# Kernel tuning notes

Hardware: AMD Instinct MI355X
Metric: run time of the kernel (lower is better)

The kernel has to match this reference:

```python
import jax, jax.numpy as jnp
import numpy as np

B, S, DIN, D, H, DK, FF, V, L = 4, 1024, 768, 224, 8, 28, 600, 8000, 8


def setup_inputs() -> dict:
    key = jax.random.key(0)
    ks = iter(jax.random.split(key, 32))
    g = lambda shape, s=0.02: jax.random.normal(next(ks), shape, jnp.float32) * s
    return {
        "x": jax.random.normal(next(ks), (B, S, DIN), jnp.float32),
        "Wp": g((DIN, D)), "bp": jnp.zeros((D,), jnp.float32),
        # per-layer stacked params, leading axis = L layers
        "Wq": g((L, H, D, DK)), "bq": jnp.zeros((L, H, DK), jnp.float32),
        "Wk": g((L, H, D, DK)), "bk": jnp.zeros((L, H, DK), jnp.float32),
        "Wv": g((L, H, D, DK)), "bv": jnp.zeros((L, H, DK), jnp.float32),
        "Wo": g((L, D, D)), "bo": jnp.zeros((L, D), jnp.float32),
        "W1": g((L, D, FF)), "b1": jnp.zeros((L, FF), jnp.float32),
        "W2": g((L, FF, FF)), "b2": jnp.zeros((L, FF), jnp.float32),
        "W3": g((L, FF, D)), "b3": jnp.zeros((L, D), jnp.float32),
        # LayerNorm over last TWO dims (seq, dmodel), one shared instance per layer
        "lnw": jnp.ones((L, S, D), jnp.float32), "lnb": jnp.zeros((L, S, D), jnp.float32),
        "Wf": g((D, V)), "bf": jnp.zeros((V,), jnp.float32),
    }


def _pos_enc(S_, D_):
    pos = jnp.arange(S_, dtype=jnp.float32)[:, None]          # [S,1]
    i = jnp.arange(D_, dtype=jnp.float32)[None, :]            # [1,D]
    ang = pos / jnp.power(jnp.float32(10000.0), 2.0 * i / D_)  # uses 2*i for BOTH
    return jnp.where(jnp.arange(D_)[None, :] % 2 == 0, jnp.sin(ang), jnp.cos(ang))


def _ln2d(x, w, b):
    # LayerNorm over last two dims (seq, dmodel), eps=1e-5
    mu = jnp.mean(x, axis=(-2, -1), keepdims=True)
    var = jnp.var(x, axis=(-2, -1), keepdims=True)
    return (x - mu) / jnp.sqrt(var + 1e-5) * w + b


def _attn(x, Wq, bq, Wk, bk, Wv, bv, Wo, bo):
    q = jnp.einsum('bsd,hdk->bhsk', x, Wq) + bq[:, None, :]
    k = jnp.einsum('bsd,hdk->bhsk', x, Wk) + bk[:, None, :]
    v = jnp.einsum('bsd,hdk->bhsk', x, Wv) + bv[:, None, :]
    scores = jnp.einsum('bhqk,bhsk->bhqs', q, k) / jnp.sqrt(jnp.float32(DK))
    causal = jnp.tril(jnp.ones((S, S), bool))
    scores = jnp.where(causal, scores, -jnp.inf)
    a = jax.nn.softmax(scores, axis=-1)
    o = jnp.einsum('bhqs,bhsk->bqhk', a, v).reshape(x.shape[0], S, D)
    return o @ Wo + bo + x  # residual inside attention (as in source)


def reference(x, Wp, bp, Wq, bq, Wk, bk, Wv, bv, Wo, bo,
              W1, b1, W2, b2, W3, b3, lnw, lnb, Wf, bf):
    h = x @ Wp + bp                      # proj_to_224: [B,S,224]
    h = h + _pos_enc(S, D)[None]         # positional encoding
    for l in range(L):
        h = _attn(h, Wq[l], bq[l], Wk[l], bk[l], Wv[l], bv[l], Wo[l], bo[l])
        h = _ln2d(h, lnw[l], lnb[l])
        f = jax.nn.relu(h @ W1[l] + b1[l])
        f = jax.nn.relu(f @ W2[l] + b2[l])
        f = f @ W3[l] + b3[l]
        h = _ln2d(f + h, lnw[l], lnb[l])  # feed_forward's LN (same params)
        h = _ln2d(h, lnw[l], lnb[l])      # outer LN (same params again)
    logits = (h @ Wf + bf) / 1.0          # temperature = 1.0
    return jax.nn.softmax(logits, axis=2)
```

## Files before the change

### kernel.cpp

```cpp
#include <hip/hip_runtime.h>
#include <math.h>

#define GF_BIAS   1
#define GF_RELU   2
#define GF_RESID  4
#define GF_POSENC 8
#define GF_F32OUT 16
#define GF_STAT6  32
#define GF_SWAP   64
#define GF_LNA    128
#define GF_LNA2   256
#define GF_LNRES  512
#define GF_LNRES2 1024

namespace {
constexpr int BB = 4, SS = 1024, DD = 224, FFF = 600, VV = 8000, LLl = 8;
constexpr int SD = SS * DD;
constexpr float INV_SD = 1.0f / (float)SD;

constexpr size_t WP   = 0;
constexpr size_t WQKV = WP + (size_t)256 * 768;
constexpr size_t WO   = WQKV + (size_t)LLl * 704 * 256;
constexpr size_t W1T  = WO + (size_t)LLl * 256 * 256;
constexpr size_t W2T  = W1T + (size_t)LLl * 640 * 256;
constexpr size_t W3T  = W2T + (size_t)LLl * 640 * 640;
constexpr size_t WFT  = W3T + (size_t)LLl * 256 * 640;
constexpr size_t HB   = WFT + (size_t)8064 * 256;
constexpr size_t H2B  = HB + (size_t)4096 * 256;
constexpr size_t OBUF = H2B + (size_t)4096 * 256;
constexpr size_t BIG  = OBUF + (size_t)4096 * 256;
constexpr size_t ENDB = BIG + (size_t)2 * 4096 * 640;
constexpr size_t FBYTE = ENDB * 2;
}

using short8 = __attribute__((ext_vector_type(8))) short;
using f32x4  = __attribute__((ext_vector_type(4))) float;

__device__ __forceinline__ float bits2f(unsigned u) {
  union { unsigned u; float f; } v; v.u = u; return v.f;
}
__device__ __forceinline__ unsigned short f2b(float f) {
  union { float f; unsigned u; } v; v.f = f;
  unsigned r = v.u + 0x7FFFu + ((v.u >> 16) & 1u);
  return (unsigned short)(r >> 16);
}
__device__ __forceinline__ float b2f(unsigned short b) {
  return bits2f((unsigned)b << 16);
}

__device__ __forceinline__ uint4 ln8(uint4 raw, const float* __restrict__ wp,
                                     const float* __restrict__ bp,
                                     float mu1, float rs1, float mu2, float rs2,
                                     bool dbl) {
  float4 w0 = *(const float4*)wp, w1v = *(const float4*)(wp + 4);
  float4 b0 = *(const float4*)bp, b1v = *(const float4*)(bp + 4);
  float wv[8] = {w0.x, w0.y, w0.z, w0.w, w1v.x, w1v.y, w1v.z, w1v.w};
  float bv[8] = {b0.x, b0.y, b0.z, b0.w, b1v.x, b1v.y, b1v.z, b1v.w};
  const unsigned* u = (const unsigned*)&raw;
  uint4 out;
  unsigned* ou = (unsigned*)&out;
#pragma unroll
  for (int q = 0; q < 4; ++q) {
    float x0 = bits2f(u[q] << 16), x1 = bits2f(u[q] & 0xFFFF0000u);
    float y0 = (x0 - mu1) * rs1 * wv[q * 2] + bv[q * 2];
    float y1 = (x1 - mu1) * rs1 * wv[q * 2 + 1] + bv[q * 2 + 1];
    if (dbl) {
      y0 = (y0 - mu2) * rs2 * wv[q * 2] + bv[q * 2];
      y1 = (y1 - mu2) * rs2 * wv[q * 2 + 1] + bv[q * 2 + 1];
    }
    ou[q] = (unsigned)f2b(y0) | ((unsigned)f2b(y1) << 16);
  }
  return out;
}

template <int BM, int BN, int FLAGS>
__global__ __launch_bounds__(256) void gemm_mfma(
    const unsigned short* __restrict__ A, const unsigned short* __restrict__ Bt,
    const float* __restrict__ bias, const unsigned short* __restrict__ Rz,
    void* __restrict__ Cout, int Kp, int N, int ldc,
    const float* __restrict__ lnwT, const float* __restrict__ lnbT,
    const float* __restrict__ stIn, const float* __restrict__ cst,
    const float* __restrict__ lnwS, const float* __restrict__ lnbS,
    float* __restrict__ statOut)
{
  constexpr bool HASLNA = (FLAGS & (GF_LNA | GF_LNA2)) != 0;
  constexpr bool HASLNR = (FLAGS & (GF_LNRES | GF_LNRES2)) != 0;
  constexpr bool DBLA = (FLAGS & GF_LNA2) != 0;
  constexpr bool DBLR = (FLAGS & GF_LNRES2) != 0;
  constexpr int MR = BM / 32, NR = BN / 32;
  constexpr int APT = BM / 32, BPT = BN / 32;
  constexpr int ABY = BM * 128, BBY = BN * 128;
  constexpr int CBY = (FLAGS & GF_F32OUT) ? (64 * (BN + 4) * 4) : (BM * (BN + 8) * 2);
  constexpr int SBY = (ABY + BBY) > CBY ? (ABY + BBY) : CBY;
  __shared__ __align__(16) char smem[SBY];
  __shared__ float red6[24];
  unsigned short* sA = (unsigned short*)smem;
  unsigned short* sB = (unsigned short*)(smem + ABY);
  const int t = threadIdx.x;
  const int l = t & 63;
  const int w = t >> 6, wr = w >> 1, wc = w & 1;
  const int m0 = ((FLAGS & GF_SWAP) ? blockIdx.x : blockIdx.y) * BM;
  const int n0 = ((FLAGS & GF_SWAP) ? blockIdx.y : blockIdx.x) * BN;
  const int nk = Kp >> 6;

  float mu1 = 0.f, rs1 = 1.f, mu2 = 0.f, rs2 = 1.f;
  if constexpr (HASLNA || HASLNR) {
    const float* st = stIn + (m0 >> 10) * 6;
    const float s0 = st[0], s1 = st[1];
    mu1 = s0 * INV_SD;
    rs1 = rsqrtf(s1 * INV_SD - mu1 * mu1 + 1e-5f);
    if constexpr (DBLA || DBLR) {
      const float swx = st[2], sw2x = st[3], sw2x2 = st[4], swbx = st[5];
      mu2 = (rs1 * (swx - mu1 * cst[0]) + cst[2]) * INV_SD;
      const float ey2 = (rs1 * rs1 * (sw2x2 - 2.f * mu1 * sw2x + mu1 * mu1 * cst[1]) +
                         2.f * rs1 * (swbx - mu1 * cst[4]) + cst[3]) * INV_SD;
      rs2 = rsqrtf(ey2 - mu2 * mu2 + 1e-5f);
    }
  }

  int aoff[APT], ar[APT], ac[APT];
#pragma unroll
  for (int p = 0; p < APT; ++p) {
    int off = (t + p * 256) * 16;
    int r = off >> 7;
    int cb = (off & 127) ^ ((r & 7) << 4);
    aoff[p] = off; ar[p] = r; ac[p] = cb >> 1;
  }
  int boff[BPT], br[BPT], bc[BPT];
#pragma unroll
  for (int p = 0; p < BPT; ++p) {
    int off = (t + p * 256) * 16;
    int r = off >> 7;
    int cb = (off & 127) ^ ((r & 7) << 4);
    boff[p] = off; br[p] = r; bc[p] = cb >> 1;
  }

  const unsigned short* Ab = A + (size_t)m0 * Kp;
  const unsigned short* Bb = Bt + (size_t)n0 * Kp;

  auto loadA = [&](int p, int kb) -> uint4 {
    const int d0 = kb + ac[p];
    uint4 raw = *(const uint4*)(Ab + (size_t)ar[p] * Kp + d0);
    if constexpr (HASLNA) {
      if (d0 >= DD) return make_uint4(0u, 0u, 0u, 0u);
      const int srow = (m0 + ar[p]) & (SS - 1);
      raw = ln8(raw, lnwT + (size_t)srow * DD + d0, lnbT + (size_t)srow * DD + d0,
                mu1, rs1, mu2, rs2, DBLA);
    }
    return raw;
  };

  uint4 ra[APT], rb[BPT];
#pragma unroll
  for (int p = 0; p < APT; ++p) ra[p] = loadA(p, 0);
#pragma unroll
  for (int p = 0; p < BPT; ++p) rb[p] = *(const uint4*)(Bb + (size_t)br[p] * Kp + bc[p]);

  f32x4 acc[MR][NR];
#pragma unroll
  for (int i = 0; i < MR; ++i)
#pragma unroll
    for (int j = 0; j < NR; ++j) acc[i][j] = {0.f, 0.f, 0.f, 0.f};

  for (int kt = 0; kt < nk; ++kt) {
#pragma unroll
    for (int p = 0; p < APT; ++p) *(uint4*)((char*)sA + aoff[p]) = ra[p];
#pragma unroll
    for (int p = 0; p < BPT; ++p) *(uint4*)((char*)sB + boff[p]) = rb[p];
    __syncthreads();
    if (kt + 1 < nk) {
      const int k1 = (kt + 1) * 64;
#pragma unroll
      for (int p = 0; p < APT; ++p) ra[p] = loadA(p, k1);
#pragma unroll
      for (int p = 0; p < BPT; ++p) rb[p] = *(const uint4*)(Bb + (size_t)br[p] * Kp + k1 + bc[p]);
    }
#pragma unroll
    for (int kh = 0; kh < 2; ++kh) {
      short8 af[MR], bfg[NR];
#pragma unroll
      for (int mi = 0; mi < MR; ++mi) {
        const int row = wr * (BM / 2) + mi * 16 + (l & 15);
        const int byte = (row * 128 + kh * 64 + (l >> 4) * 16) ^ ((row & 7) << 4);
        af[mi] = *(const short8*)((const char*)sA + byte);
      }
#pragma unroll
      for (int ni = 0; ni < NR; ++ni) {
        const int row = wc * (BN / 2) + ni * 16 + (l & 15);
        const int byte = (row * 128 + kh * 64 + (l >> 4) * 16) ^ ((row & 7) << 4);
        bfg[ni] = *(const short8*)((const char*)sB + byte);
      }
#pragma unroll
      for (int mi = 0; mi < MR; ++mi)
#pragma unroll
        for (int ni = 0; ni < NR; ++ni)
          acc[mi][ni] = __builtin_amdgcn_mfma_f32_16x16x32_bf16(af[mi], bfg[ni], acc[mi][ni], 0, 0, 0);
    }
    __syncthreads();
  }

  const int cl = l & 15, rl0 = (l >> 4) * 4;

  if constexpr ((FLAGS & GF_F32OUT) != 0) {
    constexpr int CST = BN + 4;
    float* Cs = (float*)smem;
    constexpr int NCH = BM / 64;
#pragma unroll
    for (int c = 0; c < NCH; ++c) {
      __syncthreads();
      if ((wr * (BM / 2)) / 64 == c) {
#pragma unroll
        for (int mi = 0; mi < MR; ++mi)
#pragma unroll
          for (int ni = 0; ni < NR; ++ni)
#pragma unroll
            for (int j = 0; j < 4; ++j) {
              const int rl = wr * (BM / 2) + mi * 16 + rl0 + j - c * 64;
              const int cc = wc * (BN / 2) + ni * 16 + cl;
              const int gn = n0 + cc;
              float v = acc[mi][ni][j];
              if ((FLAGS & GF_BIAS) && gn < N) v += bias[gn];
              Cs[rl * CST + cc] = v;
            }
      }
      __syncthreads();
      constexpr int CPR = BN / 4;
      constexpr int NIT = (64 * CPR) / 256;
#pragma unroll
      for (int i = 0; i < NIT; ++i) {
        const int ch = i * 256 + t;
        const int rr = ch / CPR, c4 = ch % CPR;
        const int gn = n0 + c4 * 4;
        const size_t gmr = (size_t)(m0 + c * 64 + rr);
        if (gn + 3 < N) {
          *(float4*)&((float*)Cout)[gmr * ldc + gn] = *(const float4*)&Cs[rr * CST + c4 * 4];
        } else {
#pragma unroll
          for (int c2 = 0; c2 < 4; ++c2)
            if (gn + c2 < N) ((float*)Cout)[gmr * ldc + gn + c2] = Cs[rr * CST + c4 * 4 + c2];
        }
      }
    }
  } else {
    constexpr int CST = BN + 8;
    unsigned short* Cs = (unsigned short*)smem;
    float ls0 = 0.f, ls1 = 0.f, ls2 = 0.f, ls3 = 0.f, ls4 = 0.f, ls5 = 0.f;
#pragma unroll
    for (int mi = 0; mi < MR; ++mi)
#pragma unroll
      for (int ni = 0; ni < NR; ++ni)
#pragma unroll
        for (int j = 0; j < 4; ++j) {
          const int rl = wr * (BM / 2) + mi * 16 + rl0 + j;
          const int cc = wc * (BN / 2) + ni * 16 + cl;
          const int gm = m0 + rl, gn = n0 + cc;
          const int srow = gm & (SS - 1);
          float v = acc[mi][ni][j];
          if ((FLAGS & GF_BIAS) && gn < N) v += bias[gn];
          if constexpr ((FLAGS & GF_RESID) != 0) {
            if constexpr (HASLNR) {
              if (gn < N) {
                float rv = b2f(Rz[(size_t)gm * ldc + gn]);
                const float wE = lnwT[(size_t)srow * DD + gn];
                const float bE = lnbT[(size_t)srow * DD + gn];
                rv = (rv - mu1) * rs1 * wE + bE;
                if constexpr (DBLR) rv = (rv - mu2) * rs2 * wE + bE;
                v += rv;
              }
            } else {
              v += b2f(Rz[(size_t)gm * ldc + gn]);
            }
          }
          if ((FLAGS & GF_POSENC) && gn < N) {
            float freq = expf(-(2.0f * gn / 224.0f) * 9.210340371976184f);
            float ang = (float)srow * freq;
            v += (gn & 1) ? cosf(ang) : sinf(ang);
          }
          if (FLAGS & GF_RELU) v = fmaxf(v, 0.f);
          if constexpr ((FLAGS & GF_STAT6) != 0) {
            if (gn < N) {
              const float wS = lnwS[(size_t)srow * DD + gn];
              const float bS = lnbS[(size_t)srow * DD + gn];
              const float wv = wS * v;
              ls0 += v; ls1 += v * v; ls2 += wv; ls3 += wS * wv;
              ls4 += wv * wv; ls5 += bS * wv;
            }
          }
          Cs[rl * CST + cc] = f2b(v);
        }
    __syncthreads();
#pragma unroll
    for (int it = 0; it < BM / 32; ++it) {
      const int rr = it * 32 + (t >> 3), qq = t & 7;
      const size_t gm = (size_t)(m0 + rr);
      *(uint4*)&((unsigned short*)Cout)[gm * ldc + n0 + qq * 8] =
          *(const uint4*)&Cs[rr * CST + qq * 8];
    }
    if constexpr ((FLAGS & GF_STAT6) != 0) {
      float s[6] = {ls0, ls1, ls2, ls3, ls4, ls5};
#pragma unroll
      for (int o2 = 32; o2 > 0; o2 >>= 1)
#pragma unroll
        for (int j = 0; j < 6; ++j) s[j] += __shfl_down(s[j], o2);
      if (l == 0)
#pragma unroll
        for (int j = 0; j < 6; ++j) red6[w * 6 + j] = s[j];
      __syncthreads();
      if (t < 6) {
        const float tot = red6[t] + red6[6 + t] + red6[12 + t] + red6[18 + t];
        atomicAdd(&statOut[(m0 >> 10) * 6 + t], tot);
      }
    }
  }
}

__global__ __launch_bounds__(256) void ffn_fused(
    const unsigned short* __restrict__ h2a,
    const unsigned short* __restrict__ W1t, const unsigned short* __restrict__ W2t,
    const unsigned short* __restrict__ W3t,
    const float* __restrict__ b1, const float* __restrict__ b2,
    const float* __restrict__ b3,
    const float* __restrict__ lnw, const float* __restrict__ lnb,
    const float* __restrict__ stA, float* __restrict__ statOut,
    unsigned short* __restrict__ Xout)
{
  __shared__ __align__(16) unsigned short sA[16 * 280];
  __shared__ __align__(16) unsigned short f1s[16 * 648];
  __shared__ __align__(16) unsigned short f2s[16 * 648];
  __shared__ float red6[24];
  const int t = threadIdx.x;
  const int l = t & 63, w = t >> 6;
  const int cl = l & 15, g8 = (l >> 4) * 8, rl0 = (l >> 4) * 4;
  const int m0 = blockIdx.x * 16;
  const float* st = stA + (m0 >> 10) * 6;
  const float mu1 = st[0] * INV_SD;
  const float rs1 = rsqrtf(st[1] * INV_SD - mu1 * mu1 + 1e-5f);

  for (int c = t; c < 512; c += 256) {
    const int r = c >> 5, col = (c & 31) * 8;
    uint4 v = make_uint4(0u, 0u, 0u, 0u);
    if (col < DD) {
      const int srow = (m0 + r) & (SS - 1);
      uint4 raw = *(const uint4*)(h2a + (size_t)(m0 + r) * 256 + col);
      v = ln8(raw, lnw + (size_t)srow * DD + col, lnb + (size_t)srow * DD + col,
              mu1, rs1, 0.f, 1.f, false);
    }
    *(uint4*)(sA + r * 280 + col) = v;
  }
  __syncthreads();

  {
    f32x4 acc[10];
#pragma unroll
    for (int i = 0; i < 10; ++i) acc[i] = {0.f, 0.f, 0.f, 0.f};
    for (int ks = 0; ks < 8; ++ks) {
      const short8 af = *(const short8*)(sA + cl * 280 + ks * 32 + g8);
#pragma unroll
      for (int ni = 0; ni < 10; ++ni) {
        const int n = w * 160 + ni * 16 + cl;
        const short8 bf = *(const short8*)(W1t + (size_t)n * 256 + ks * 32 + g8);
        acc[ni] = __builtin_amdgcn_mfma_f32_16x16x32_bf16(af, bf, acc[ni], 0, 0, 0);
      }
    }
#pragma unroll
    for (int ni = 0; ni < 10; ++ni) {
      const int col = w * 160 + ni * 16 + cl;
      const float bias = (col < FFF) ? b1[col] : 0.f;
#pragma unroll
      for (int j = 0; j < 4; ++j)
        f1s[(rl0 + j) * 648 + col] = f2b(fmaxf(acc[ni][j] + bias, 0.f));
    }
  }
  __syncthreads();

  {
    f32x4 acc[10];
#pragma unroll
    for (int i = 0; i < 10; ++i) acc[i] = {0.f, 0.f, 0.f, 0.f};
    for (int ks = 0; ks < 20; ++ks) {
      const short8 af = *(const short8*)(f1s + cl * 648 + ks * 32 + g8);
#pragma unroll
      for (int ni = 0; ni < 10; ++ni) {
        const int n = w * 160 + ni * 16 + cl;
        const short8 bf = *(const short8*)(W2t + (size_t)n * 640 + ks * 32 + g8);
        acc[ni] = __builtin_amdgcn_mfma_f32_16x16x32_bf16(af, bf, acc[ni], 0, 0, 0);
      }
    }
#pragma unroll
    for (int ni = 0; ni < 10; ++ni) {
      const int col = w * 160 + ni * 16 + cl;
      const float bias = (col < FFF) ? b2[col] : 0.f;
#pragma unroll
      for (int j = 0; j < 4; ++j)
        f2s[(rl0 + j) * 648 + col] = f2b(fmaxf(acc[ni][j] + bias, 0.f));
    }
  }
  __syncthreads();

  float s6[6] = {0.f, 0.f, 0.f, 0.f, 0.f, 0.f};
  {
    f32x4 acc[4];
#pragma unroll
    for (int i = 0; i < 4; ++i) acc[i] = {0.f, 0.f, 0.f, 0.f};
    for (int ks = 0; ks < 20; ++ks) {
      const short8 af = *(const short8*)(f2s + cl * 648 + ks * 32 + g8);
#pragma unroll
      for (int ni = 0; ni < 4; ++ni) {
        const int n = w * 64 + ni * 16 + cl;
        const short8 bf = *(const short8*)(W3t + (size_t)n * 640 + ks * 32 + g8);
        acc[ni] = __builtin_amdgcn_mfma_f32_16x16x32_bf16(af, bf, acc[ni], 0, 0, 0);
      }
    }
    unsigned short* Cs = sA;
#pragma unroll
    for (int ni = 0; ni < 4; ++ni) {
      const int col = w * 64 + ni * 16 + cl;
      const float bias = (col < DD) ? b3[col] : 0.f;
#pragma unroll
      for (int j = 0; j < 4; ++j) {
        const int gm = m0 + rl0 + j;
        const int srow = gm & (SS - 1);
        float v = acc[ni][j] + bias;
        if (col < DD) {
          const float wE = lnw[(size_t)srow * DD + col];
          const float bE = lnb[(size_t)srow * DD + col];
          v += (b2f(h2a[(size_t)gm * 256 + col]) - mu1) * rs1 * wE + bE;
          const float wv = wE * v;
          s6[0] += v; s6[1] += v * v; s6[2] += wv; s6[3] += wE * wv;
          s6[4] += wv * wv; s6[5] += bE * wv;
        }
        Cs[(rl0 + j) * 280 + col] = f2b(v);
      }
    }
  }
#pragma unroll
  for (int o2 = 32; o2 > 0; o2 >>= 1)
#pragma unroll
    for (int j2 = 0; j2 < 6; ++j2) s6[j2] += __shfl_down(s6[j2], o2);
  if (l == 0)
#pragma unroll
    for (int j2 = 0; j2 < 6; ++j2) red6[w * 6 + j2] = s6[j2];
  __syncthreads();
  if (t < 6)
    atomicAdd(&statOut[(m0 >> 10) * 6 + t],
              red6[t] + red6[6 + t] + red6[12 + t] + red6[18 + t]);
  for (int c = t; c < 512; c += 256) {
    const int r = c >> 5, col = (c & 31) * 8;
    *(uint4*)(Xout + (size_t)(m0 + r) * 256 + col) = *(const uint4*)(sA + r * 280 + col);
  }
}

__global__ void zero_stats(float* __restrict__ st)
{
  if (threadIdx.x < 424) st[threadIdx.x] = 0.f;
}

__global__ __launch_bounds__(256) void lnconst(const float* __restrict__ lnw,
                                               const float* __restrict__ lnb,
                                               float* __restrict__ cst)
{
  const int ll = blockIdx.y, g = blockIdx.x;
  const float* wv = lnw + (size_t)ll * SD + g * 3584;
  const float* bv = lnb + (size_t)ll * SD + g * 3584;
  float s[5] = {0.f, 0.f, 0.f, 0.f, 0.f};
  for (int c = threadIdx.x * 4; c < 3584; c += 1024) {
    float4 w4 = *(const float4*)(wv + c);
    float4 b4 = *(const float4*)(bv + c);
    const float* wf = (const float*)&w4;
    const float* bf2 = (const float*)&b4;
#pragma unroll
    for (int e = 0; e < 4; ++e) {
      const float ww = wf[e], bb = bf2[e];
      s[0] += ww; s[1] += ww * ww; s[2] += bb; s[3] += bb * bb; s[4] += ww * bb;
    }
  }
#pragma unroll
  for (int o2 = 32; o2 > 0; o2 >>= 1)
#pragma unroll
    for (int j = 0; j < 5; ++j) s[j] += __shfl_down(s[j], o2);
  __shared__ float red[4][5];
  if ((threadIdx.x & 63) == 0)
#pragma unroll
    for (int j = 0; j < 5; ++j) red[threadIdx.x >> 6][j] = s[j];
  __syncthreads();
  if (threadIdx.x < 5) {
    const float tot = red[0][threadIdx.x] + red[1][threadIdx.x] +
                      red[2][threadIdx.x] + red[3][threadIdx.x];
    atomicAdd(&cst[ll * 5 + threadIdx.x], tot);
  }
}

__global__ __launch_bounds__(256) void ln2mat(
    const unsigned short* __restrict__ X, const float* __restrict__ lnw,
    const float* __restrict__ lnb, const float* __restrict__ st,
    const float* __restrict__ cst, unsigned short* __restrict__ Y)
{
  const int chunk = blockIdx.x * 256 + threadIdx.x;
  const int r = chunk >> 5, cc = chunk & 31;
  if (cc >= 28) {
    *(uint4*)(Y + (size_t)r * 256 + cc * 8) = make_uint4(0u, 0u, 0u, 0u);
    return;
  }
  const int b = r >> 10, srow = r & 1023;
  const float* s = st + b * 6;
  const float mu1 = s[0] * INV_SD;
  const float rs1 = rsqrtf(s[1] * INV_SD - mu1 * mu1 + 1e-5f);
  const float mu2 = (rs1 * (s[2] - mu1 * cst[0]) + cst[2]) * INV_SD;
  const float ey2 = (rs1 * rs1 * (s[4] - 2.f * mu1 * s[3] + mu1 * mu1 * cst[1]) +
                     2.f * rs1 * (s[5] - mu1 * cst[4]) + cst[3]) * INV_SD;
  const float rs2 = rsqrtf(ey2 - mu2 * mu2 + 1e-5f);
  uint4 raw = *(const uint4*)(X + (size_t)r * 256 + cc * 8);
  uint4 out = ln8(raw, lnw + (size_t)srow * DD + cc * 8, lnb + (size_t)srow * DD + cc * 8,
                  mu1, rs1, mu2, rs2, true);
  *(uint4*)(Y + (size_t)r * 256 + cc * 8) = out;
}

__global__ __launch_bounds__(256) void prep_wt2(
    const float* __restrict__ W, unsigned short* __restrict__ O,
    int K, int N, int Kp, int Np, size_t sW, size_t sO)
{
  const int ll = blockIdx.y;
  const int tx = Np >> 5;
  const int tn = blockIdx.x % tx, tk = blockIdx.x / tx;
  const int n0 = tn * 32, k0 = tk * 32;
  const float* Wl = W + sW * ll;
  unsigned short* Ol = O + sO * ll;
  __shared__ float T[32][36];
  {
    const int r = threadIdx.x >> 3, c4 = (threadIdx.x & 7) * 4;
    const int k = k0 + r, n = n0 + c4;
    float4 v = make_float4(0.f, 0.f, 0.f, 0.f);
    if (k < K) {
      if (n + 3 < N) v = *(const float4*)&Wl[(size_t)k * N + n];
      else {
        if (n + 0 < N) v.x = Wl[(size_t)k * N + n + 0];
        if (n + 1 < N) v.y = Wl[(size_t)k * N + n + 1];
        if (n + 2 < N) v.z = Wl[(size_t)k * N + n + 2];
        if (n + 3 < N) v.w = Wl[(size_t)k * N + n + 3];
      }
    }
    *(float4*)&T[r][c4] = v;
  }
  __syncthreads();
  {
    const int nl = threadIdx.x >> 3, k4 = (threadIdx.x & 7) * 4;
    ushort4 u;
    u.x = f2b(T[k4 + 0][nl]); u.y = f2b(T[k4 + 1][nl]);
    u.z = f2b(T[k4 + 2][nl]); u.w = f2b(T[k4 + 3][nl]);
    *(ushort4*)&Ol[(size_t)(n0 + nl) * Kp + k0 + k4] = u;
  }
}

__global__ void prep_wqkv(const float* __restrict__ Wq, const float* __restrict__ Wk,
                          const float* __restrict__ Wv, const float* __restrict__ bq,
                          const float* __restrict__ bk, const float* __restrict__ bv,
                          unsigned short* __restrict__ O, float* __restrict__ bcat)
{
  const int idx = blockIdx.x * 256 + threadIdx.x;
  if (idx < LLl * 8 * 224 * 28) {
    const int kk = idx % 28;
    const int d  = (idx / 28) % 224;
    const int h  = (idx / (28 * 224)) % 8;
    const int ll = idx / (28 * 224 * 8);
    const int col = h * 28 + kk;
    const size_t base = (size_t)ll * (704 * 256);
    O[base + (size_t)col * 256 + d]         = f2b(Wq[idx]);
    O[base + (size_t)(224 + col) * 256 + d] = f2b(Wk[idx]);
    O[base + (size_t)(448 + col) * 256 + d] = f2b(Wv[idx]);
  }
  if (idx < LLl * 8 * 28) {
    const int kk = idx % 28;
    const int h  = (idx / 28) % 8;
    const int ll = idx / (28 * 8);
    const int col = h * 28 + kk;
    bcat[ll * 672 + col]       = bq[idx];
    bcat[ll * 672 + 224 + col] = bk[idx];
    bcat[ll * 672 + 448 + col] = bv[idx];
  }
}

__global__ void prep_x(const float* __restrict__ x, unsigned short* __restrict__ xb)
{
  const size_t i = ((size_t)blockIdx.x * 256 + threadIdx.x) * 4;
  float4 v = *(const float4*)(x + i);
  ushort4 o;
  o.x = f2b(v.x); o.y = f2b(v.y); o.z = f2b(v.z); o.w = f2b(v.w);
  *(ushort4*)(xb + i) = o;
}

__global__ __launch_bounds__(256) void attn_mfma(const unsigned short* __restrict__ qkv,
                                                 unsigned short* __restrict__ o)
{
  const int bh = blockIdx.x;
  const int qt = (int)gridDim.y - 1 - (int)blockIdx.y;
  const int b = bh >> 3, h = bh & 7;
  const int tid = threadIdx.x;
  const int w = tid >> 6, l = tid & 63;
  const int cl = l & 15, g = l >> 4;
  const int qbase = qt * 64 + w * 16;
  const float scale = 0.1889822365046136f;

  __shared__ unsigned short Ks[32 * 40];
  __shared__ unsigned short Vt[32 * 40];
  __shared__ unsigned short Ps[4][16 * 40];

  short8 aq;
  {
    const unsigned short* qp = qkv + ((size_t)(b * SS + qbase + cl)) * 704 + h * 28;
#pragma unroll
    for (int e = 0; e < 8; ++e) {
      const int d = g * 8 + e;
      ((unsigned short*)&aq)[e] = (d < 28) ? qp[d] : (unsigned short)0;
    }
  }

  f32x4 o0 = {0.f, 0.f, 0.f, 0.f}, o1 = {0.f, 0.f, 0.f, 0.f};
  float m[4] = {-INFINITY, -INFINITY, -INFINITY, -INFINITY};
  float lsum[4] = {0.f, 0.f, 0.f, 0.f};

  const int ntiles = qt * 2 + 2;
  const int ntw = ((qbase + 15) >> 5) + 1;

  const int sr = tid >> 3, sc4 = (tid & 7) << 2;
  const bool sact = (sc4 < 28);
  ushort4 ku = make_ushort4(0, 0, 0, 0), vu = make_ushort4(0, 0, 0, 0);
  if (sact) {
    const unsigned short* kp = qkv + ((size_t)(b * SS + sr)) * 704 + 224 + h * 28 + sc4;
    ku = *(const ushort4*)kp;
    vu = *(const ushort4*)(kp + 224);
  }

  for (int tile = 0; tile < ntiles; ++tile) {
    const int t0 = tile * 32;
    __syncthreads();
    *(ushort4*)&Ks[sr * 40 + sc4] = ku;
    Vt[(sc4 + 0) * 40 + sr] = vu.x;
    Vt[(sc4 + 1) * 40 + sr] = vu.y;
    Vt[(sc4 + 2) * 40 + sr] = vu.z;
    Vt[(sc4 + 3) * 40 + sr] = vu.w;
    __syncthreads();
    if (tile + 1 < ntiles && sact) {
      const unsigned short* kp =
          qkv + ((size_t)(b * SS + (tile + 1) * 32 + sr)) * 704 + 224 + h * 28 + sc4;
      ku = *(const ushort4*)kp;
      vu = *(const ushort4*)(kp + 224);
    }
    if (tile >= ntw) continue;

    const short8 bk0 = *(const short8*)&Ks[cl * 40 + g * 8];
    const short8 bk1 = *(const short8*)&Ks[(cl + 16) * 40 + g * 8];
    f32x4 zz = {0.f, 0.f, 0.f, 0.f};
    f32x4 s0 = __builtin_amdgcn_mfma_f32_16x16x32_bf16(aq, bk0, zz, 0, 0, 0);
    f32x4 s1 = __builtin_amdgcn_mfma_f32_16x16x32_bf16(aq, bk1, zz, 0, 0, 0);

    const bool diag = (t0 + 31 > qbase);
#pragma unroll
    for (int jj = 0; jj < 4; ++jj) {
      float v0 = s0[jj] * scale, v1 = s1[jj] * scale;
      if (diag) {
        const int qr = qbase + g * 4 + jj;
        if (t0 + cl > qr)      v0 = -INFINITY;
        if (t0 + 16 + cl > qr) v1 = -INFINITY;
      }
      float rm = fmaxf(v0, v1);
      rm = fmaxf(rm, __shfl_xor(rm, 1));
      rm = fmaxf(rm, __shfl_xor(rm, 2));
      rm = fmaxf(rm, __shfl_xor(rm, 4));
      rm = fmaxf(rm, __shfl_xor(rm, 8));
      const float mnew = fmaxf(m[jj], rm);
      const float r2 = __expf(m[jj] - mnew);
      m[jj] = mnew;
      const float e0 = __expf(v0 - mnew), e1 = __expf(v1 - mnew);
      lsum[jj] = lsum[jj] * r2 + e0 + e1;
      o0[jj] *= r2; o1[jj] *= r2;
      Ps[w][(g * 4 + jj) * 40 + cl]      = f2b(e0);
      Ps[w][(g * 4 + jj) * 40 + cl + 16] = f2b(e1);
    }
    const short8 pa  = *(const short8*)&Ps[w][cl * 40 + g * 8];
    const short8 bv0 = *(const short8*)&Vt[cl * 40 + g * 8];
    const short8 bv1 = *(const short8*)&Vt[(cl + 16) * 40 + g * 8];
    o0 = __builtin_amdgcn_mfma_f32_16x16x32_bf16(pa, bv0, o0, 0, 0, 0);
    o1 = __builtin_amdgcn_mfma_f32_16x16x32_bf16(pa, bv1, o1, 0, 0, 0);
  }

#pragma unroll
  for (int jj = 0; jj < 4; ++jj) {
    float ls = lsum[jj];
    ls += __shfl_xor(ls, 1);
    ls += __shfl_xor(ls, 2);
    ls += __shfl_xor(ls, 4);
    ls += __shfl_xor(ls, 8);
    const float inv = 1.0f / ls;
    const int row = qbase + g * 4 + jj;
    unsigned short* op = o + ((size_t)(b * SS + row)) * 256 + h * 28;
    op[cl] = f2b(o0[jj] * inv);
    if (cl < 12) op[16 + cl] = f2b(o1[jj] * inv);
  }
}

__global__ __launch_bounds__(256) void softmax_rows(float* __restrict__ logits)
{
  const int row = blockIdx.x;
  float* p = logits + (size_t)row * VV;
  __shared__ float buf[VV];
  __shared__ float red[4];
  const int tid = threadIdx.x;

  float mx = -INFINITY;
  for (int i = tid; i < VV; i += 256) { float v = p[i]; buf[i] = v; mx = fmaxf(mx, v); }
#pragma unroll
  for (int o2 = 32; o2 > 0; o2 >>= 1) mx = fmaxf(mx, __shfl_down(mx, o2));
  if ((tid & 63) == 0) red[tid >> 6] = mx;
  __syncthreads();
  mx = fmaxf(fmaxf(red[0], red[1]), fmaxf(red[2], red[3]));
  __syncthreads();

  float s = 0.f;
  for (int i = tid; i < VV; i += 256) { float e = __expf(buf[i] - mx); buf[i] = e; s += e; }
#pragma unroll
  for (int o2 = 32; o2 > 0; o2 >>= 1) s += __shfl_down(s, o2);
  if ((tid & 63) == 0) red[tid >> 6] = s;
  __syncthreads();
  s = red[0] + red[1] + red[2] + red[3];
  const float inv = 1.0f / s;
  for (int i = tid; i < VV; i += 256) p[i] = buf[i] * inv;
}

extern "C" void kernel_launch(void* const* d_in, const int* in_sizes, int n_in,
                              void* d_out, int out_size, void* d_ws, size_t ws_size,
                              hipStream_t stream) {
  const float* x   = (const float*)d_in[0];
  const float* Wp  = (const float*)d_in[1];
  const float* bp  = (const float*)d_in[2];
  const float* Wq  = (const float*)d_in[3];
  const float* bq  = (const float*)d_in[4];
  const float* Wk  = (const float*)d_in[5];
  const float* bk  = (const float*)d_in[6];
  const float* Wv  = (const float*)d_in[7];
  const float* bv  = (const float*)d_in[8];
  const float* Wo  = (const float*)d_in[9];
  const float* bo  = (const float*)d_in[10];
  const float* W1  = (const float*)d_in[11];
  const float* b1  = (const float*)d_in[12];
  const float* W2  = (const float*)d_in[13];
  const float* b2  = (const float*)d_in[14];
  const float* W3  = (const float*)d_in[15];
  const float* b3  = (const float*)d_in[16];
  const float* lnw = (const float*)d_in[17];
  const float* lnb = (const float*)d_in[18];
  const float* Wf  = (const float*)d_in[19];
  const float* bf  = (const float*)d_in[20];

  unsigned short* wsb = (unsigned short*)d_ws;
  unsigned short* wpT   = wsb + WP;
  unsigned short* wqkvT = wsb + WQKV;
  unsigned short* woT   = wsb + WO;
  unsigned short* w1T   = wsb + W1T;
  unsigned short* w2T   = wsb + W2T;
  unsigned short* w3T   = wsb + W3T;
  unsigned short* wfT   = wsb + WFT;
  unsigned short* X     = wsb + HB;
  unsigned short* h2a   = wsb + H2B;
  unsigned short* obuf  = wsb + OBUF;
  unsigned short* xb    = wsb + BIG;
  unsigned short* qkvb  = wsb + BIG;
  float* bcat  = (float*)((char*)d_ws + FBYTE);
  float* stats = bcat + LLl * 672;
  float* cstA  = stats + 384;

  zero_stats<<<1, 512, 0, stream>>>(stats);
  lnconst<<<dim3(64, LLl), 256, 0, stream>>>(lnw, lnb, cstA);
  hipMemsetAsync(wqkvT, 0, (size_t)LLl * 704 * 256 * 2, stream);
  prep_x<<<3072, 256, 0, stream>>>(x, xb);
  prep_wt2<<<dim3(192, 1), 256, 0, stream>>>(Wp, wpT, 768, 224, 768, 256, 0, 0);
  prep_wqkv<<<dim3(1568, 1), 256, 0, stream>>>(Wq, Wk, Wv, bq, bk, bv, wqkvT, bcat);
  prep_wt2<<<dim3(64, 8), 256, 0, stream>>>(Wo, woT, 224, 224, 256, 256,
                                            (size_t)224 * 224, (size_t)256 * 256);
  prep_wt2<<<dim3(160, 8), 256, 0, stream>>>(W1, w1T, 224, 600, 256, 640,
                                             (size_t)224 * 600, (size_t)640 * 256);
  prep_wt2<<<dim3(400, 8), 256, 0, stream>>>(W2, w2T, 600, 600, 640, 640,
                                             (size_t)600 * 600, (size_t)640 * 640);
  prep_wt2<<<dim3(160, 8), 256, 0, stream>>>(W3, w3T, 600, 224, 640, 256,
                                             (size_t)600 * 224, (size_t)256 * 640);
  prep_wt2<<<dim3(2016, 1), 256, 0, stream>>>(Wf, wfT, 224, 8000, 256, 8064, 0, 0);

  gemm_mfma<32, 64, GF_BIAS | GF_POSENC><<<dim3(4, 128), 256, 0, stream>>>(
      xb, wpT, bp, nullptr, X, 768, 224, 256,
      nullptr, nullptr, nullptr, nullptr, nullptr, nullptr, nullptr);

  for (int l = 0; l < LLl; ++l) {
    float* stA = stats + (size_t)(2 * l) * 24;
    float* stB = stats + (size_t)(2 * l + 1) * 24;
    const float* stPrev = stats + (size_t)(2 * l - 1) * 24;
    const float* lnwP = lnw + (size_t)(l - 1) * SD;
    const float* lnbP = lnb + (size_t)(l - 1) * SD;
    const float* cstP = cstA + (l - 1) * 5;
    const float* lnwL = lnw + (size_t)l * SD;
    const float* lnbL = lnb + (size_t)l * SD;

    if (l == 0) {
      gemm_mfma<64, 64, GF_BIAS><<<dim3(11, 64), 256, 0, stream>>>(
          X, wqkvT, bcat, nullptr, qkvb, 256, 672, 704,
          nullptr, nullptr, nullptr, nullptr, nullptr, nullptr, nullptr);
    } else {
      gemm_mfma<64, 64, GF_BIAS | GF_LNA2><<<dim3(11, 64), 256, 0, stream>>>(
          X, wqkvT + (size_t)l * 704 * 256, bcat + l * 672, nullptr, qkvb, 256, 672, 704,
          lnwP, lnbP, stPrev, cstP, nullptr, nullptr, nullptr);
    }
    attn_mfma<<<dim3(BB * 8, SS / 64), 256, 0, stream>>>(qkvb, obuf);
    if (l == 0) {
      gemm_mfma<32, 64, GF_BIAS | GF_RESID | GF_STAT6><<<dim3(4, 128), 256, 0, stream>>>(
          obuf, woT, bo, X, h2a, 256, 224, 256,
          nullptr, nullptr, nullptr, nullptr, lnwL, lnbL, stA);
    } else {
      gemm_mfma<32, 64, GF_BIAS | GF_RESID | GF_LNRES2 | GF_STAT6>
          <<<dim3(4, 128), 256, 0, stream>>>(
          obuf, woT + (size_t)l * 256 * 256, bo + (size_t)l * 224, X, h2a, 256, 224, 256,
          lnwP, lnbP, stPrev, cstP, lnwL, lnbL, stA);
    }
    ffn_fused<<<256, 256, 0, stream>>>(
        h2a, w1T + (size_t)l * 640 * 256, w2T + (size_t)l * 640 * 640,
        w3T + (size_t)l * 256 * 640, b1 + (size_t)l * 600, b2 + (size_t)l * 600,
        b3 + (size_t)l * 224, lnwL, lnbL, stA, stB, X);
  }

  ln2mat<<<512, 256, 0, stream>>>(X, lnw + (size_t)7 * SD, lnb + (size_t)7 * SD,
                                  stats + (size_t)15 * 24, cstA + 7 * 5, h2a);
  gemm_mfma<128, 128, GF_BIAS | GF_F32OUT | GF_SWAP><<<dim3(32, 63), 256, 0, stream>>>(
      h2a, wfT, bf, nullptr, (float*)d_out, 256, 8000, 8000,
      nullptr, nullptr, nullptr, nullptr, nullptr, nullptr, nullptr);
  softmax_rows<<<4096, 256, 0, stream>>>((float*)d_out);
}
```

Baseline: 1.274 ms.

## Merge prep kernels, widen FFN blocks, fuse final LN, vectorize softmax

Folds the separate weight-transpose, LN-constant and stat-zeroing launches into one prep_weights kernel, and moves the stat zeroing into prep_x, to cut launch count. ffn_fused now runs 512 threads (8 waves) per block, each covering half as many output columns, to add latency hiding. The standalone ln2mat pass is removed and the final LayerNorm is applied inside the vocab GEMM's A-load through GF_LNA2. softmax_rows switches to float4 loads and stores. Risks: stat zeroing in block 0 of prep_x must finish before the atomics in prep_weights that accumulate into cstA (which sits inside the zeroed range), and LNA2 in the large GEMM recomputes the normalization for every N tile.

```diff
diff --git a/kernel.cpp b/kernel.cpp
--- a/kernel.cpp
+++ b/kernel.cpp
@@ -314,7 +314,7 @@
   }
 }
 
-__global__ __launch_bounds__(256) void ffn_fused(
+__global__ __launch_bounds__(512) void ffn_fused(
     const unsigned short* __restrict__ h2a,
     const unsigned short* __restrict__ W1t, const unsigned short* __restrict__ W2t,
     const unsigned short* __restrict__ W3t,
@@ -327,7 +327,7 @@
   __shared__ __align__(16) unsigned short sA[16 * 280];
   __shared__ __align__(16) unsigned short f1s[16 * 648];
   __shared__ __align__(16) unsigned short f2s[16 * 648];
-  __shared__ float red6[24];
+  __shared__ float red6[48];
   const int t = threadIdx.x;
   const int l = t & 63, w = t >> 6;
   const int cl = l & 15, g8 = (l >> 4) * 8, rl0 = (l >> 4) * 4;
@@ -336,8 +336,8 @@
   const float mu1 = st[0] * INV_SD;
   const float rs1 = rsqrtf(st[1] * INV_SD - mu1 * mu1 + 1e-5f);
 
-  for (int c = t; c < 512; c += 256) {
-    const int r = c >> 5, col = (c & 31) * 8;
+  {
+    const int r = t >> 5, col = (t & 31) * 8;
     uint4 v = make_uint4(0u, 0u, 0u, 0u);
     if (col < DD) {
       const int srow = (m0 + r) & (SS - 1);
@@ -350,21 +350,21 @@
   __syncthreads();
 
   {
-    f32x4 acc[10];
-#pragma unroll
-    for (int i = 0; i < 10; ++i) acc[i] = {0.f, 0.f, 0.f, 0.f};
+    f32x4 acc[5];
+#pragma unroll
+    for (int i = 0; i < 5; ++i) acc[i] = {0.f, 0.f, 0.f, 0.f};
     for (int ks = 0; ks < 8; ++ks) {
       const short8 af = *(const short8*)(sA + cl * 280 + ks * 32 + g8);
 #pragma unroll
-      for (int ni = 0; ni < 10; ++ni) {
-        const int n = w * 160 + ni * 16 + cl;
+      for (int ni = 0; ni < 5; ++ni) {
+        const int n = w * 80 + ni * 16 + cl;
         const short8 bf = *(const short8*)(W1t + (size_t)n * 256 + ks * 32 + g8);
         acc[ni] = __builtin_amdgcn_mfma_f32_16x16x32_bf16(af, bf, acc[ni], 0, 0, 0);
       }
     }
 #pragma unroll
-    for (int ni = 0; ni < 10; ++ni) {
-      const int col = w * 160 + ni * 16 + cl;
+    for (int ni = 0; ni < 5; ++ni) {
+      const int col = w * 80 + ni * 16 + cl;
       const float bias = (col < FFF) ? b1[col] : 0.f;
 #pragma unroll
       for (int j = 0; j < 4; ++j)
@@ -374,21 +374,21 @@
   __syncthreads();
 
   {
-    f32x4 acc[10];
-#pragma unroll
-    for (int i = 0; i < 10; ++i) acc[i] = {0.f, 0.f, 0.f, 0.f};
+    f32x4 acc[5];
+#pragma unroll
+    for (int i = 0; i < 5; ++i) acc[i] = {0.f, 0.f, 0.f, 0.f};
     for (int ks = 0; ks < 20; ++ks) {
       const short8 af = *(const short8*)(f1s + cl * 648 + ks * 32 + g8);
 #pragma unroll
-      for (int ni = 0; ni < 10; ++ni) {
-        const int n = w * 160 + ni * 16 + cl;
+      for (int ni = 0; ni < 5; ++ni) {
+        const int n = w * 80 + ni * 16 + cl;
         const short8 bf = *(const short8*)(W2t + (size_t)n * 640 + ks * 32 + g8);
         acc[ni] = __builtin_amdgcn_mfma_f32_16x16x32_bf16(af, bf, acc[ni], 0, 0, 0);
       }
     }
 #pragma unroll
-    for (int ni = 0; ni < 10; ++ni) {
-      const int col = w * 160 + ni * 16 + cl;
+    for (int ni = 0; ni < 5; ++ni) {
+      const int col = w * 80 + ni * 16 + cl;
       const float bias = (col < FFF) ? b2[col] : 0.f;
 #pragma unroll
       for (int j = 0; j < 4; ++j)
@@ -399,22 +399,22 @@
 
   float s6[6] = {0.f, 0.f, 0.f, 0.f, 0.f, 0.f};
   {
-    f32x4 acc[4];
-#pragma unroll
-    for (int i = 0; i < 4; ++i) acc[i] = {0.f, 0.f, 0.f, 0.f};
+    f32x4 acc[2];
+#pragma unroll
+    for (int i = 0; i < 2; ++i) acc[i] = {0.f, 0.f, 0.f, 0.f};
     for (int ks = 0; ks < 20; ++ks) {
       const short8 af = *(const short8*)(f2s + cl * 648 + ks * 32 + g8);
 #pragma unroll
-      for (int ni = 0; ni < 4; ++ni) {
-        const int n = w * 64 + ni * 16 + cl;
+      for (int ni = 0; ni < 2; ++ni) {
+        const int n = w * 32 + ni * 16 + cl;
         const short8 bf = *(const short8*)(W3t + (size_t)n * 640 + ks * 32 + g8);
         acc[ni] = __builtin_amdgcn_mfma_f32_16x16x32_bf16(af, bf, acc[ni], 0, 0, 0);
       }
     }
     unsigned short* Cs = sA;
 #pragma unroll
-    for (int ni = 0; ni < 4; ++ni) {
-      const int col = w * 64 + ni * 16 + cl;
+    for (int ni = 0; ni < 2; ++ni) {
+      const int col = w * 32 + ni * 16 + cl;
       const float bias = (col < DD) ? b3[col] : 0.f;
 #pragma unroll
       for (int j = 0; j < 4; ++j) {
@@ -441,91 +441,28 @@
 #pragma unroll
     for (int j2 = 0; j2 < 6; ++j2) red6[w * 6 + j2] = s6[j2];
   __syncthreads();
-  if (t < 6)
-    atomicAdd(&statOut[(m0 >> 10) * 6 + t],
-              red6[t] + red6[6 + t] + red6[12 + t] + red6[18 + t]);
-  for (int c = t; c < 512; c += 256) {
-    const int r = c >> 5, col = (c & 31) * 8;
+  if (t < 6) {
+    float tot = 0.f;
+#pragma unroll
+    for (int ww = 0; ww < 8; ++ww) tot += red6[ww * 6 + t];
+    atomicAdd(&statOut[(m0 >> 10) * 6 + t], tot);
+  }
+  {
+    const int r = t >> 5, col = (t & 31) * 8;
     *(uint4*)(Xout + (size_t)(m0 + r) * 256 + col) = *(const uint4*)(sA + r * 280 + col);
   }
 }
 
-__global__ void zero_stats(float* __restrict__ st)
+__device__ __forceinline__ void prep_wt2_body(
+    const float* __restrict__ W, unsigned short* __restrict__ O,
+    int K, int N, int Kp, int Np, size_t sW, size_t sO, int tile, int ll,
+    float* __restrict__ T )
 {
-  if (threadIdx.x < 424) st[threadIdx.x] = 0.f;
-}
-
-__global__ __launch_bounds__(256) void lnconst(const float* __restrict__ lnw,
-                                               const float* __restrict__ lnb,
-                                               float* __restrict__ cst)
-{
-  const int ll = blockIdx.y, g = blockIdx.x;
-  const float* wv = lnw + (size_t)ll * SD + g * 3584;
-  const float* bv = lnb + (size_t)ll * SD + g * 3584;
-  float s[5] = {0.f, 0.f, 0.f, 0.f, 0.f};
-  for (int c = threadIdx.x * 4; c < 3584; c += 1024) {
-    float4 w4 = *(const float4*)(wv + c);
-    float4 b4 = *(const float4*)(bv + c);
-    const float* wf = (const float*)&w4;
-    const float* bf2 = (const float*)&b4;
-#pragma unroll
-    for (int e = 0; e < 4; ++e) {
-      const float ww = wf[e], bb = bf2[e];
-      s[0] += ww; s[1] += ww * ww; s[2] += bb; s[3] += bb * bb; s[4] += ww * bb;
-    }
-  }
-#pragma unroll
-  for (int o2 = 32; o2 > 0; o2 >>= 1)
-#pragma unroll
-    for (int j = 0; j < 5; ++j) s[j] += __shfl_down(s[j], o2);
-  __shared__ float red[4][5];
-  if ((threadIdx.x & 63) == 0)
-#pragma unroll
-    for (int j = 0; j < 5; ++j) red[threadIdx.x >> 6][j] = s[j];
-  __syncthreads();
-  if (threadIdx.x < 5) {
-    const float tot = red[0][threadIdx.x] + red[1][threadIdx.x] +
-                      red[2][threadIdx.x] + red[3][threadIdx.x];
-    atomicAdd(&cst[ll * 5 + threadIdx.x], tot);
-  }
-}
-
-__global__ __launch_bounds__(256) void ln2mat(
-    const unsigned short* __restrict__ X, const float* __restrict__ lnw,
-    const float* __restrict__ lnb, const float* __restrict__ st,
-    const float* __restrict__ cst, unsigned short* __restrict__ Y)
-{
-  const int chunk = blockIdx.x * 256 + threadIdx.x;
-  const int r = chunk >> 5, cc = chunk & 31;
-  if (cc >= 28) {
-    *(uint4*)(Y + (size_t)r * 256 + cc * 8) = make_uint4(0u, 0u, 0u, 0u);
-    return;
-  }
-  const int b = r >> 10, srow = r & 1023;
-  const float* s = st + b * 6;
-  const float mu1 = s[0] * INV_SD;
-  const float rs1 = rsqrtf(s[1] * INV_SD - mu1 * mu1 + 1e-5f);
-  const float mu2 = (rs1 * (s[2] - mu1 * cst[0]) + cst[2]) * INV_SD;
-  const float ey2 = (rs1 * rs1 * (s[4] - 2.f * mu1 * s[3] + mu1 * mu1 * cst[1]) +
-                     2.f * rs1 * (s[5] - mu1 * cst[4]) + cst[3]) * INV_SD;
-  const float rs2 = rsqrtf(ey2 - mu2 * mu2 + 1e-5f);
-  uint4 raw = *(const uint4*)(X + (size_t)r * 256 + cc * 8);
-  uint4 out = ln8(raw, lnw + (size_t)srow * DD + cc * 8, lnb + (size_t)srow * DD + cc * 8,
-                  mu1, rs1, mu2, rs2, true);
-  *(uint4*)(Y + (size_t)r * 256 + cc * 8) = out;
-}
-
-__global__ __launch_bounds__(256) void prep_wt2(
-    const float* __restrict__ W, unsigned short* __restrict__ O,
-    int K, int N, int Kp, int Np, size_t sW, size_t sO)
-{
-  const int ll = blockIdx.y;
   const int tx = Np >> 5;
-  const int tn = blockIdx.x % tx, tk = blockIdx.x / tx;
+  const int tn = tile % tx, tk = tile / tx;
   const int n0 = tn * 32, k0 = tk * 32;
   const float* Wl = W + sW * ll;
   unsigned short* Ol = O + sO * ll;
-  __shared__ float T[32][36];
   {
     const int r = threadIdx.x >> 3, c4 = (threadIdx.x & 7) * 4;
     const int k = k0 + r, n = n0 + c4;
@@ -539,15 +476,81 @@
         if (n + 3 < N) v.w = Wl[(size_t)k * N + n + 3];
       }
     }
-    *(float4*)&T[r][c4] = v;
+    *(float4*)&T[r * 36 + c4] = v;
   }
   __syncthreads();
   {
     const int nl = threadIdx.x >> 3, k4 = (threadIdx.x & 7) * 4;
     ushort4 u;
-    u.x = f2b(T[k4 + 0][nl]); u.y = f2b(T[k4 + 1][nl]);
-    u.z = f2b(T[k4 + 2][nl]); u.w = f2b(T[k4 + 3][nl]);
+    u.x = f2b(T[(k4 + 0) * 36 + nl]); u.y = f2b(T[(k4 + 1) * 36 + nl]);
+    u.z = f2b(T[(k4 + 2) * 36 + nl]); u.w = f2b(T[(k4 + 3) * 36 + nl]);
     *(ushort4*)&Ol[(size_t)(n0 + nl) * Kp + k0 + k4] = u;
+  }
+}
+
+__global__ __launch_bounds__(256) void prep_weights(
+    const float* __restrict__ Wp, const float* __restrict__ Wo,
+    const float* __restrict__ W1, const float* __restrict__ W2,
+    const float* __restrict__ W3, const float* __restrict__ Wf,
+    const float* __restrict__ lnw, const float* __restrict__ lnb,
+    unsigned short* __restrict__ wpT, unsigned short* __restrict__ woT,
+    unsigned short* __restrict__ w1T, unsigned short* __restrict__ w2T,
+    unsigned short* __restrict__ w3T, unsigned short* __restrict__ wfT,
+    float* __restrict__ cst)
+{
+  __shared__ float T[32 * 36];
+  const int b = blockIdx.x;
+  if (b < 192) {
+    prep_wt2_body(Wp, wpT, 768, 224, 768, 256, 0, 0, b, 0, T);
+  } else if (b < 704) {
+    const int f = b - 192;
+    prep_wt2_body(Wo, woT, 224, 224, 256, 256, (size_t)224 * 224, (size_t)256 * 256,
+                  f % 64, f / 64, T);
+  } else if (b < 1984) {
+    const int f = b - 704;
+    prep_wt2_body(W1, w1T, 224, 600, 256, 640, (size_t)224 * 600, (size_t)640 * 256,
+                  f % 160, f / 160, T);
+  } else if (b < 5184) {
+    const int f = b - 1984;
+    prep_wt2_body(W2, w2T, 600, 600, 640, 640, (size_t)600 * 600, (size_t)640 * 640,
+                  f % 400, f / 400, T);
+  } else if (b < 6464) {
+    const int f = b - 5184;
+    prep_wt2_body(W3, w3T, 600, 224, 640, 256, (size_t)600 * 224, (size_t)256 * 640,
+                  f % 160, f / 160, T);
+  } else if (b < 8480) {
+    prep_wt2_body(Wf, wfT, 224, 8000, 256, 8064, 0, 0, b - 6464, 0, T);
+  } else {
+    const int f = b - 8480;
+    const int g = f & 63, ll = f >> 6;
+    const float* wv = lnw + (size_t)ll * SD + g * 3584;
+    const float* bv = lnb + (size_t)ll * SD + g * 3584;
+    float s[5] = {0.f, 0.f, 0.f, 0.f, 0.f};
+    for (int c = threadIdx.x * 4; c < 3584; c += 1024) {
+      float4 w4 = *(const float4*)(wv + c);
+      float4 b4 = *(const float4*)(bv + c);
+      const float* wf2 = (const float*)&w4;
+      const float* bf2 = (const float*)&b4;
+#pragma unroll
+      for (int e = 0; e < 4; ++e) {
+        const float ww = wf2[e], bb = bf2[e];
+        s[0] += ww; s[1] += ww * ww; s[2] += bb; s[3] += bb * bb; s[4] += ww * bb;
+      }
+    }
+#pragma unroll
+    for (int o2 = 32; o2 > 0; o2 >>= 1)
+#pragma unroll
+      for (int j = 0; j < 5; ++j) s[j] += __shfl_down(s[j], o2);
+    float* red = T;
+    if ((threadIdx.x & 63) == 0)
+#pragma unroll
+      for (int j = 0; j < 5; ++j) red[(threadIdx.x >> 6) * 5 + j] = s[j];
+    __syncthreads();
+    if (threadIdx.x < 5) {
+      const float tot = red[threadIdx.x] + red[5 + threadIdx.x] +
+                        red[10 + threadIdx.x] + red[15 + threadIdx.x];
+      atomicAdd(&cst[ll * 5 + threadIdx.x], tot);
+    }
   }
 }
 
@@ -579,8 +582,12 @@
   }
 }
 
-__global__ void prep_x(const float* __restrict__ x, unsigned short* __restrict__ xb)
+__global__ void prep_x(const float* __restrict__ x, unsigned short* __restrict__ xb,
+                       float* __restrict__ st)
 {
+  if (blockIdx.x == 0) {
+    for (int i = threadIdx.x; i < 424; i += 256) st[i] = 0.f;
+  }
   const size_t i = ((size_t)blockIdx.x * 256 + threadIdx.x) * 4;
   float4 v = *(const float4*)(x + i);
   ushort4 o;
@@ -702,12 +709,16 @@
 {
   const int row = blockIdx.x;
   float* p = logits + (size_t)row * VV;
-  __shared__ float buf[VV];
+  __shared__ float4 buf[VV / 4];
   __shared__ float red[4];
   const int tid = threadIdx.x;
 
   float mx = -INFINITY;
-  for (int i = tid; i < VV; i += 256) { float v = p[i]; buf[i] = v; mx = fmaxf(mx, v); }
+  for (int i = tid; i < VV / 4; i += 256) {
+    float4 v = *(const float4*)(p + i * 4);
+    buf[i] = v;
+    mx = fmaxf(fmaxf(fmaxf(mx, v.x), fmaxf(v.y, v.z)), v.w);
+  }
 #pragma unroll
   for (int o2 = 32; o2 > 0; o2 >>= 1) mx = fmaxf(mx, __shfl_down(mx, o2));
   if ((tid & 63) == 0) red[tid >> 6] = mx;
@@ -716,14 +727,24 @@
   __syncthreads();
 
   float s = 0.f;
-  for (int i = tid; i < VV; i += 256) { float e = __expf(buf[i] - mx); buf[i] = e; s += e; }
+  for (int i = tid; i < VV / 4; i += 256) {
+    float4 v = buf[i];
+    v.x = __expf(v.x - mx); v.y = __expf(v.y - mx);
+    v.z = __expf(v.z - mx); v.w = __expf(v.w - mx);
+    buf[i] = v;
+    s += v.x + v.y + v.z + v.w;
+  }
 #pragma unroll
   for (int o2 = 32; o2 > 0; o2 >>= 1) s += __shfl_down(s, o2);
   if ((tid & 63) == 0) red[tid >> 6] = s;
   __syncthreads();
   s = red[0] + red[1] + red[2] + red[3];
   const float inv = 1.0f / s;
-  for (int i = tid; i < VV; i += 256) p[i] = buf[i] * inv;
+  for (int i = tid; i < VV / 4; i += 256) {
+    float4 v = buf[i];
+    v.x *= inv; v.y *= inv; v.z *= inv; v.w *= inv;
+    *(float4*)(p + i * 4) = v;
+  }
 }
 
 extern "C" void kernel_launch(void* const* d_in, const int* in_sizes, int n_in,
@@ -768,21 +789,11 @@
   float* stats = bcat + LLl * 672;
   float* cstA  = stats + 384;
 
-  zero_stats<<<1, 512, 0, stream>>>(stats);
-  lnconst<<<dim3(64, LLl), 256, 0, stream>>>(lnw, lnb, cstA);
   hipMemsetAsync(wqkvT, 0, (size_t)LLl * 704 * 256 * 2, stream);
-  prep_x<<<3072, 256, 0, stream>>>(x, xb);
-  prep_wt2<<<dim3(192, 1), 256, 0, stream>>>(Wp, wpT, 768, 224, 768, 256, 0, 0);
-  prep_wqkv<<<dim3(1568, 1), 256, 0, stream>>>(Wq, Wk, Wv, bq, bk, bv, wqkvT, bcat);
-  prep_wt2<<<dim3(64, 8), 256, 0, stream>>>(Wo, woT, 224, 224, 256, 256,
-                                            (size_t)224 * 224, (size_t)256 * 256);
-  prep_wt2<<<dim3(160, 8), 256, 0, stream>>>(W1, w1T, 224, 600, 256, 640,
-                                             (size_t)224 * 600, (size_t)640 * 256);
-  prep_wt2<<<dim3(400, 8), 256, 0, stream>>>(W2, w2T, 600, 600, 640, 640,
-                                             (size_t)600 * 600, (size_t)640 * 640);
-  prep_wt2<<<dim3(160, 8), 256, 0, stream>>>(W3, w3T, 600, 224, 640, 256,
-                                             (size_t)600 * 224, (size_t)256 * 640);
-  prep_wt2<<<dim3(2016, 1), 256, 0, stream>>>(Wf, wfT, 224, 8000, 256, 8064, 0, 0);
+  prep_x<<<3072, 256, 0, stream>>>(x, xb, stats);
+  prep_wqkv<<<1568, 256, 0, stream>>>(Wq, Wk, Wv, bq, bk, bv, wqkvT, bcat);
+  prep_weights<<<8992, 256, 0, stream>>>(Wp, Wo, W1, W2, W3, Wf, lnw, lnb,
+                                         wpT, woT, w1T, w2T, w3T, wfT, cstA);
 
   gemm_mfma<32, 64, GF_BIAS | GF_POSENC><<<dim3(4, 128), 256, 0, stream>>>(
       xb, wpT, bp, nullptr, X, 768, 224, 256,
@@ -818,16 +829,16 @@
           obuf, woT + (size_t)l * 256 * 256, bo + (size_t)l * 224, X, h2a, 256, 224, 256,
           lnwP, lnbP, stPrev, cstP, lnwL, lnbL, stA);
     }
-    ffn_fused<<<256, 256, 0, stream>>>(
+    ffn_fused<<<256, 512, 0, stream>>>(
         h2a, w1T + (size_t)l * 640 * 256, w2T + (size_t)l * 640 * 640,
         w3T + (size_t)l * 256 * 640, b1 + (size_t)l * 600, b2 + (size_t)l * 600,
         b3 + (size_t)l * 224, lnwL, lnbL, stA, stB, X);
   }
 
-  ln2mat<<<512, 256, 0, stream>>>(X, lnw + (size_t)7 * SD, lnb + (size_t)7 * SD,
-                                  stats + (size_t)15 * 24, cstA + 7 * 5, h2a);
-  gemm_mfma<128, 128, GF_BIAS | GF_F32OUT | GF_SWAP><<<dim3(32, 63), 256, 0, stream>>>(
-      h2a, wfT, bf, nullptr, (float*)d_out, 256, 8000, 8000,
-      nullptr, nullptr, nullptr, nullptr, nullptr, nullptr, nullptr);
+  gemm_mfma<128, 128, GF_BIAS | GF_F32OUT | GF_SWAP | GF_LNA2>
+      <<<dim3(32, 63), 256, 0, stream>>>(
+      X, wfT, bf, nullptr, (float*)d_out, 256, 8000, 8000,
+      lnw + (size_t)7 * SD, lnb + (size_t)7 * SD, stats + (size_t)15 * 24,
+      cstA + 7 * 5, nullptr, nullptr, nullptr);
   softmax_rows<<<4096, 256, 0, stream>>>((float*)d_out);
 }
```

Result: faster. 1.219 ms (-4.3%).
